# Kernel tuning notes

Hardware: AMD Instinct MI355X
Metric: run time of the kernel (lower is better)

Reference implementation:

```python
import jax, jax.numpy as jnp
import numpy as np

EPS = 1e-5
INF = 1e9
H, D = 16, 24  # no_heads, c_hidden

def layer_norm(x, w, b):
    mu = jnp.mean(x, axis=-1, keepdims=True)
    var = jnp.mean(jnp.square(x - mu), axis=-1, keepdims=True)
    return (x - mu) * jax.lax.rsqrt(var + EPS) * w + b

def setup_inputs() -> dict:
    key = jax.random.key(0)
    ks = jax.random.split(key, 12)
    B, N, Cq, Cz = 1, 1024, 384, 128
    s = 0.02
    return {
        "a": jax.random.normal(ks[0], (B, N, Cq), jnp.float32),
        "z": jax.random.normal(ks[1], (B, N, N, Cz), jnp.float32),
        "mask": jnp.ones((B, N), jnp.float32),
        "ln_a_w": jnp.ones((Cq,), jnp.float32),
        "ln_a_b": jnp.zeros((Cq,), jnp.float32),
        "ln_z_w": jnp.ones((Cz,), jnp.float32),
        "ln_z_b": jnp.zeros((Cz,), jnp.float32),
        "w_z": jax.random.normal(ks[2], (Cz, H), jnp.float32) * s,
        "wq": jax.random.normal(ks[3], (Cq, H * D), jnp.float32) * s,
        "wk": jax.random.normal(ks[4], (Cq, H * D), jnp.float32) * s,
        "wv": jax.random.normal(ks[5], (Cq, H * D), jnp.float32) * s,
        "wg": jax.random.normal(ks[6], (Cq, H * D), jnp.float32) * s,
        "bg": jnp.ones((H * D,), jnp.float32),
        "wo": jax.random.normal(ks[7], (H * D, Cq), jnp.float32) * s,
        "bo": jnp.zeros((Cq,), jnp.float32),
    }

def reference(a, z, mask, ln_a_w, ln_a_b, ln_z_w, ln_z_b, w_z, wq, wk, wv, wg, bg, wo, bo):
    B, N, Cq = a.shape
    a_ln = layer_norm(a, ln_a_w, ln_a_b)                      # [B,N,Cq]
    # pair bias: LN -> Linear(no bias) -> permute to [B,H,N,N]
    zb = layer_norm(z, ln_z_w, ln_z_b) @ w_z                  # [B,N,N,H]
    pair_bias = jnp.transpose(zb, (0, 3, 1, 2))               # [B,H,N,N]
    mask_bias = (INF * (mask - 1.0))[:, None, None, :]        # [B,1,1,N]
    q = (a_ln @ wq).reshape(B, N, H, D) * (D ** -0.5)
    k = (a_ln @ wk).reshape(B, N, H, D)
    v = (a_ln @ wv).reshape(B, N, H, D)
    logits = jnp.einsum("bqhd,bkhd->bhqk", q, k) + mask_bias + pair_bias
    attn = jax.nn.softmax(logits, axis=-1)
    o = jnp.einsum("bhqk,bkhd->bqhd", attn, v)                # [B,N,H,D]
    g = jax.nn.sigmoid(a_ln @ wg + bg).reshape(B, N, H, D)
    o = (g * o).reshape(B, N, H * D)
    return o @ wo + bo
```

## Files before the change

kernel.cpp:

```cpp
#include <hip/hip_runtime.h>
#include <hip/hip_bf16.h>

typedef float f32x4 __attribute__((ext_vector_type(4)));
typedef short s16x8 __attribute__((ext_vector_type(8)));

__device__ __forceinline__ unsigned short f2bf(float x){
  unsigned u = __float_as_uint(x);
  u += 0x7fffu + ((u >> 16) & 1u);
  return (unsigned short)(u >> 16);
}
__device__ __forceinline__ float bf2f(unsigned short h){
  return __uint_as_float(((unsigned)h) << 16);
}
__device__ __forceinline__ unsigned pk_bf(float a, float b){
  __hip_bfloat162 t = __float22bfloat162_rn(make_float2(a, b));
  return *reinterpret_cast<unsigned*>(&t);
}

__global__ __launch_bounds__(256) void prep_kernel(const float* __restrict__ a, const float* __restrict__ ln_a_w,
                             const float* __restrict__ ln_a_b, const float* __restrict__ lnzw,
                             const float* __restrict__ lnzb, const float* __restrict__ w_z,
                             const float* __restrict__ wq, const float* __restrict__ wk,
                             const float* __restrict__ wv, const float* __restrict__ wg,
                             const float* __restrict__ wo,
                             unsigned short* __restrict__ a_lnB, unsigned short* __restrict__ wBall,
                             unsigned short* __restrict__ wwB, float* __restrict__ TU,
                             unsigned short* __restrict__ qTp, unsigned short* __restrict__ kTp,
                             unsigned short* __restrict__ vTt){
  int bid = blockIdx.x, tid = threadIdx.x;
  if (bid < 180){
    __shared__ float t[64][65];
    int mat = bid/36, tt = bid - mat*36;
    int c0 = (tt % 6)*64, k0 = (tt / 6)*64;
    const float* src = mat == 0 ? wq : mat == 1 ? wk : mat == 2 ? wv : mat == 3 ? wg : wo;
    int r = tid >> 4, c4 = (tid & 15)*4;
    #pragma unroll
    for (int rr = 0; rr < 4; ++rr){
      float4 v = *(const float4*)(src + (size_t)(k0 + r + rr*16)*384 + c0 + c4);
      t[r + rr*16][c4+0] = v.x; t[r + rr*16][c4+1] = v.y;
      t[r + rr*16][c4+2] = v.z; t[r + rr*16][c4+3] = v.w;
    }
    __syncthreads();
    float scale = (mat == 0) ? 0.20412414523193154f : 1.f;
    int cc = tid >> 2, kp = (tid & 3)*16;
    unsigned ow[8];
    #pragma unroll
    for (int j = 0; j < 8; ++j)
      ow[j] = pk_bf(t[kp + 2*j][cc]*scale, t[kp + 2*j + 1][cc]*scale);
    unsigned short* dst = wBall + ((size_t)(mat*384 + c0 + cc)*384 + k0 + kp);
    *(uint4*)dst       = make_uint4(ow[0], ow[1], ow[2], ow[3]);
    *(uint4*)(dst + 8) = make_uint4(ow[4], ow[5], ow[6], ow[7]);
  } else if (bid < 436){
    int r = (bid - 180)*4 + (tid >> 6), l = tid & 63;
    const float* ap = a + (size_t)r*384;
    float x[6]; float s = 0.f, sq = 0.f;
    #pragma unroll
    for (int i = 0; i < 6; ++i){ x[i] = ap[i*64 + l]; s += x[i]; sq += x[i]*x[i]; }
    #pragma unroll
    for (int off = 32; off; off >>= 1){ s += __shfl_xor(s, off); sq += __shfl_xor(sq, off); }
    float mu = s*(1.f/384.f);
    float var = sq*(1.f/384.f) - mu*mu;
    float rs = rsqrtf(var + 1e-5f);
    #pragma unroll
    for (int i = 0; i < 6; ++i){ int c = i*64 + l; a_lnB[(size_t)r*384 + c] = f2bf((x[i]-mu)*rs*ln_a_w[c] + ln_a_b[c]); }
  } else if (bid == 436){
    if (tid < 128){
      float lw = lnzw[tid];
      #pragma unroll
      for (int h = 0; h < 16; ++h) wwB[tid*16 + h] = f2bf(lw * w_z[tid*16 + h]);
    }
    if (tid < 16){
      float T = 0.f, U = 0.f;
      for (int c = 0; c < 128; ++c){ T += lnzw[c]*w_z[c*16 + tid]; U += lnzb[c]*w_z[c*16 + tid]; }
      TU[tid] = T; TU[16 + tid] = U;
    }
  } else {
    int t = (bid - 437)*256 + tid;
    uint4 zv = make_uint4(0,0,0,0);
    if (t < 16384)      *(uint4*)(qTp + (size_t)t*32 + 24) = zv;
    else if (t < 32768) *(uint4*)(kTp + (size_t)(t - 16384)*32 + 24) = zv;
    else {
      int t2 = t - 32768;
      int h = t2 >> 10, w = t2 & 1023;
      *(uint4*)(vTt + ((size_t)h*32 + 24)*1024 + (size_t)w*8) = zv;
    }
  }
}

__global__ __launch_bounds__(256) void qkvg_kernel(const unsigned short* __restrict__ AB,
                                                   const unsigned short* __restrict__ wBt,
                                                   const float* __restrict__ bg,
                                                   unsigned short* __restrict__ qTp, unsigned short* __restrict__ kTp,
                                                   unsigned short* __restrict__ vTt, float* __restrict__ g){
  __shared__ short Al[64*8*8];
  __shared__ short Bl[64*8*8];
  int tid = threadIdx.x;
  int wave = tid >> 6, lane = tid & 63, l15 = lane & 15, sub = lane >> 4;
  int n0 = blockIdx.x*64, m0 = blockIdx.y*64;
  f32x4 acc[4];
  #pragma unroll
  for (int c = 0; c < 4; ++c) acc[c] = (f32x4){0.f,0.f,0.f,0.f};
  const s16x8* Ag = (const s16x8*)AB;
  const s16x8* Bg = (const s16x8*)wBt;
  s16x8* Al8 = (s16x8*)Al; s16x8* Bl8 = (s16x8*)Bl;
  for (int ks = 0; ks < 6; ++ks){
    int k0u = ks*8;
    #pragma unroll
    for (int j = 0; j < 2; ++j){
      int idx = tid*2 + j;
      int row = idx >> 3, u = idx & 7;
      Al8[row*8 + (u ^ (row & 7))] = Ag[(size_t)(m0 + row)*48 + k0u + u];
      Bl8[row*8 + (u ^ (row & 7))] = Bg[(size_t)(n0 + row)*48 + k0u + u];
    }
    __syncthreads();
    #pragma unroll
    for (int kk = 0; kk < 2; ++kk){
      int arow = wave*16 + l15;
      s16x8 af = Al8[arow*8 + ((kk*4 + sub) ^ (arow & 7))];
      #pragma unroll
      for (int c = 0; c < 4; ++c){
        int brow = c*16 + l15;
        s16x8 bf = Bl8[brow*8 + ((kk*4 + sub) ^ (brow & 7))];
        acc[c] = __builtin_amdgcn_mfma_f32_16x16x32_bf16(af, bf, acc[c], 0, 0, 0);
      }
    }
    __syncthreads();
  }
  int which = blockIdx.x / 6;
  int cb = n0 - which*384;
  if (which == 3){
    #pragma unroll
    for (int c = 0; c < 4; ++c){
      int col = cb + c*16 + l15;
      #pragma unroll
      for (int r = 0; r < 4; ++r){
        int row = m0 + wave*16 + sub*4 + r;
        float t = acc[c][r] + bg[col];
        g[(size_t)row*384 + col] = 1.f/(1.f + __expf(-t));
      }
    }
  } else if (which == 2){
    #pragma unroll
    for (int c = 0; c < 4; ++c){
      int col = cb + c*16 + l15;
      int h = col/24, d = col - h*24;
      unsigned p0 = pk_bf(acc[c][0], acc[c][1]);
      unsigned p1 = pk_bf(acc[c][2], acc[c][3]);
      size_t base = ((size_t)h*32 + d)*1024 + (size_t)(m0 + wave*16 + sub*4);
      *(uint2*)(vTt + base) = make_uint2(p0, p1);
    }
  } else {
    unsigned short* dst = which == 0 ? qTp : kTp;
    #pragma unroll
    for (int c = 0; c < 4; ++c){
      int col = cb + c*16 + l15;
      int h = col/24, d = col - h*24;
      #pragma unroll
      for (int r = 0; r < 4; ++r){
        int row = m0 + wave*16 + sub*4 + r;
        dst[((size_t)(h << 10) + row)*32 + d] = f2bf(acc[c][r]);
      }
    }
  }
}

__global__ __launch_bounds__(256) void zbias_kernel(const float* __restrict__ z, const unsigned short* __restrict__ wwB,
                                                    const float* __restrict__ TU, const float* __restrict__ mask,
                                                    unsigned short* __restrict__ pbM){
  __shared__ float sums[64];
  __shared__ float sqs[64];
  __shared__ float accT[64][17];
  int tid = threadIdx.x;
  int wave = tid >> 6, lane = tid & 63;
  int h = lane & 15, sub = lane >> 4;
  s16x8 bfr[4];
  #pragma unroll
  for (int kc = 0; kc < 4; ++kc)
    #pragma unroll
    for (int j = 0; j < 8; ++j) bfr[kc][j] = (short)wwB[(kc*32 + sub*8 + j)*16 + h];
  s16x8 ones1;
  #pragma unroll
  for (int j = 0; j < 8; ++j) ones1[j] = (h == 0) ? (short)0x3F80 : (short)0;
  int eh = tid >> 4, epl0 = (tid & 15)*4;
  float Te = TU[eh], Ue = TU[16 + eh];
  int row = wave*16 + h;
  for (int it = 0; it < 4; ++it){
    int tile = blockIdx.x + it*4096;
    size_t pairBase = (size_t)tile*64;
    const float* zrow = z + (pairBase + row)*128;
    f32x4 acc  = {0.f, 0.f, 0.f, 0.f};
    f32x4 accS = {0.f, 0.f, 0.f, 0.f};
    f32x4 accG = {0.f, 0.f, 0.f, 0.f};
    #pragma unroll
    for (int kc = 0; kc < 4; ++kc){
      f32x4 v0 = *(const f32x4*)(zrow + kc*32 + sub*8);
      f32x4 v1 = *(const f32x4*)(zrow + kc*32 + sub*8 + 4);
      union { unsigned u[4]; s16x8 s; } cv;
      cv.u[0] = pk_bf(v0.x, v0.y); cv.u[1] = pk_bf(v0.z, v0.w);
      cv.u[2] = pk_bf(v1.x, v1.y); cv.u[3] = pk_bf(v1.z, v1.w);
      s16x8 af = cv.s;
      acc  = __builtin_amdgcn_mfma_f32_16x16x32_bf16(af, bfr[kc], acc, 0, 0, 0);
      accS = __builtin_amdgcn_mfma_f32_16x16x32_bf16(af, ones1, accS, 0, 0, 0);
      accG = __builtin_amdgcn_mfma_f32_16x16x32_bf16(af, af, accG, 0, 0, 0);
    }
    #pragma unroll
    for (int r = 0; r < 4; ++r) accT[wave*16 + sub*4 + r][h] = acc[r];
    if (h == 0){
      #pragma unroll
      for (int r = 0; r < 4; ++r) sums[wave*16 + sub*4 + r] = accS[r];
    }
    if (sub == (h >> 2)){
      int r = h & 3;
      float vq = r == 0 ? accG[0] : r == 1 ? accG[1] : r == 2 ? accG[2] : accG[3];
      sqs[wave*16 + h] = vq;
    }
    __syncthreads();
    float mus[4], rss[4];
    #pragma unroll
    for (int rr = 0; rr < 4; ++rr){
      float mu = sums[epl0+rr]*(1.f/128.f);
      float var = sqs[epl0+rr]*(1.f/128.f) - mu*mu;
      mus[rr] = mu; rss[rr] = rsqrtf(var + 1e-5f);
    }
    size_t p0 = pairBase + epl0;
    int q = (int)(p0 >> 10), k0 = (int)(p0 & 1023);
    float4 mk = *(const float4*)(mask + k0);
    float bv[4];
    bv[0] = rss[0]*(accT[epl0+0][eh] - mus[0]*Te) + Ue + 1e9f*(mk.x - 1.f);
    bv[1] = rss[1]*(accT[epl0+1][eh] - mus[1]*Te) + Ue + 1e9f*(mk.y - 1.f);
    bv[2] = rss[2]*(accT[epl0+2][eh] - mus[2]*Te) + Ue + 1e9f*(mk.z - 1.f);
    bv[3] = rss[3]*(accT[epl0+3][eh] - mus[3]*Te) + Ue + 1e9f*(mk.w - 1.f);
    int qb = q >> 6, q64 = q & 63;
    int qg = q64 >> 4, subq = (q64 >> 2) & 3, rr = q64 & 3;
    int kkt = k0 >> 6, c = (k0 >> 4) & 3, l15k = k0 & 15;
    size_t cbase = ((((size_t)(eh*16 + qb)*16 + kkt)*4 + qg)*4 + c)*256 + (size_t)rr;
    #pragma unroll
    for (int i = 0; i < 4; ++i)
      pbM[cbase + (size_t)(subq*16 + l15k + i)*4] = f2bf(bv[i]);
    __syncthreads();
  }
}

__global__ __launch_bounds__(512) void attn_kernel(const unsigned short* __restrict__ qTp, const unsigned short* __restrict__ kTp,
                                                   const unsigned short* __restrict__ vTt, const unsigned short* __restrict__ pbM,
                                                   const float* __restrict__ g, unsigned short* __restrict__ ogB){
  __shared__ float lds[8192];
  int tid = threadIdx.x;
  int wave = tid >> 6, lane = tid & 63, l15 = lane & 15, sub = lane >> 4;
  int qb = blockIdx.x, h = blockIdx.y;
  int qg = wave & 3, half = wave >> 2;
  int qrow = qb*64 + qg*16 + l15;
  s16x8 qf = *(const s16x8*)(qTp + ((size_t)(h << 10) + qrow)*32 + sub*8);
  f32x4 o0 = {0.f,0.f,0.f,0.f}, o1 = {0.f,0.f,0.f,0.f};
  float m[4] = {-1e30f,-1e30f,-1e30f,-1e30f}, l[4] = {0.f,0.f,0.f,0.f};
  char* Pb = (char*)(lds + wave*1024);
  const unsigned short* kBase = kTp + ((size_t)(h << 10))*32;
  const unsigned short* vBase = vTt + (size_t)h*32*1024;
  const unsigned short* pbW = pbM + (size_t)(h*16 + qb)*16*4096 + (size_t)qg*1024 + (size_t)lane*4;
  for (int t = 0; t < 8; ++t){
    int kkt = half*8 + t;
    int kk0 = kkt*64;
    f32x4 s[4];
    #pragma unroll
    for (int c = 0; c < 4; ++c){
      s16x8 kf = *(const s16x8*)(kBase + (size_t)(kk0 + c*16 + l15)*32 + sub*8);
      s[c] = __builtin_amdgcn_mfma_f32_16x16x32_bf16(qf, kf, (f32x4){0.f,0.f,0.f,0.f}, 0, 0, 0);
    }
    const unsigned short* pbt = pbW + (size_t)kkt*4096;
    #pragma unroll
    for (int c = 0; c < 4; ++c){
      uint2 pv = *(const uint2*)(pbt + c*256);
      s[c][0] += bf2f((unsigned short)(pv.x & 0xffff));
      s[c][1] += bf2f((unsigned short)(pv.x >> 16));
      s[c][2] += bf2f((unsigned short)(pv.y & 0xffff));
      s[c][3] += bf2f((unsigned short)(pv.y >> 16));
    }
    #pragma unroll
    for (int r = 0; r < 4; ++r){
      float pm = fmaxf(fmaxf(s[0][r], s[1][r]), fmaxf(s[2][r], s[3][r]));
      pm = fmaxf(pm, __shfl_xor(pm, 1));
      pm = fmaxf(pm, __shfl_xor(pm, 2));
      pm = fmaxf(pm, __shfl_xor(pm, 4));
      pm = fmaxf(pm, __shfl_xor(pm, 8));
      float mn = fmaxf(m[r], pm);
      float corr = __expf(m[r] - mn);
      m[r] = mn;
      float ps = 0.f;
      #pragma unroll
      for (int c = 0; c < 4; ++c){ s[c][r] = __expf(s[c][r] - mn); ps += s[c][r]; }
      ps += __shfl_xor(ps, 1); ps += __shfl_xor(ps, 2);
      ps += __shfl_xor(ps, 4); ps += __shfl_xor(ps, 8);
      l[r] = l[r]*corr + ps;
      o0[r] *= corr; o1[r] *= corr;
    }
    #pragma unroll
    for (int c = 0; c < 4; ++c){
      #pragma unroll
      for (int r = 0; r < 4; ++r){
        int qq = sub*4 + r;
        int byte = ((qq*128 + (c*16 + l15)*2)) ^ ((qq & 7) << 4);
        *(short*)(Pb + byte) = (short)f2bf(s[c][r]);
      }
    }
    #pragma unroll
    for (int kh = 0; kh < 2; ++kh){
      int byteA = (l15*128 + kh*64 + sub*16) ^ ((l15 & 7) << 4);
      s16x8 pa = *(const s16x8*)(Pb + byteA);
      s16x8 vb0 = *(const s16x8*)(vBase + (size_t)l15*1024 + kk0 + kh*32 + sub*8);
      s16x8 vb1 = *(const s16x8*)(vBase + (size_t)(16 + l15)*1024 + kk0 + kh*32 + sub*8);
      o0 = __builtin_amdgcn_mfma_f32_16x16x32_bf16(pa, vb0, o0, 0, 0, 0);
      o1 = __builtin_amdgcn_mfma_f32_16x16x32_bf16(pa, vb1, o1, 0, 0, 0);
    }
  }
  {
    float* cw = lds + wave*1024 + lane*16;
    cw[0] = o0[0]; cw[1] = o0[1]; cw[2] = o0[2]; cw[3] = o0[3];
    cw[4] = o1[0]; cw[5] = o1[1]; cw[6] = o1[2]; cw[7] = o1[3];
    cw[8] = m[0]; cw[9] = m[1]; cw[10] = m[2]; cw[11] = m[3];
    cw[12] = l[0]; cw[13] = l[1]; cw[14] = l[2]; cw[15] = l[3];
  }
  __syncthreads();
  if (wave < 4){
    const float* c2 = lds + (wave + 4)*1024 + lane*16;
    #pragma unroll
    for (int r = 0; r < 4; ++r){
      float m2 = c2[8 + r], l2 = c2[12 + r];
      float nm = fmaxf(m[r], m2);
      float f1 = __expf(m[r] - nm), f2 = __expf(m2 - nm);
      float L = l[r]*f1 + l2*f2;
      float O0 = o0[r]*f1 + c2[r]*f2;
      float O1 = o1[r]*f1 + c2[4 + r]*f2;
      float inv = 1.f/L;
      int q = qb*64 + qg*16 + sub*4 + r;
      size_t base = (size_t)q*384 + h*24;
      ogB[base + l15] = f2bf(g[base + l15]*O0*inv);
      if (l15 < 8) ogB[base + 16 + l15] = f2bf(g[base + 16 + l15]*O1*inv);
    }
  }
}

__global__ __launch_bounds__(256) void gemm_out(const unsigned short* __restrict__ AB,
                                                const unsigned short* __restrict__ wBo,
                                                const float* __restrict__ bo, float* __restrict__ dst){
  __shared__ short Al[64*8*8];
  __shared__ short Bl[64*8*8];
  int tid = threadIdx.x;
  int wave = tid >> 6, lane = tid & 63, l15 = lane & 15, sub = lane >> 4;
  int n0 = blockIdx.x*64, m0 = blockIdx.y*64;
  f32x4 acc[4];
  #pragma unroll
  for (int c = 0; c < 4; ++c) acc[c] = (f32x4){0.f,0.f,0.f,0.f};
  const s16x8* Ag = (const s16x8*)AB;
  const s16x8* Bg = (const s16x8*)wBo;
  s16x8* Al8 = (s16x8*)Al; s16x8* Bl8 = (s16x8*)Bl;
  for (int ks = 0; ks < 6; ++ks){
    int k0u = ks*8;
    #pragma unroll
    for (int j = 0; j < 2; ++j){
      int idx = tid*2 + j;
      int row = idx >> 3, u = idx & 7;
      Al8[row*8 + (u ^ (row & 7))] = Ag[(size_t)(m0 + row)*48 + k0u + u];
      Bl8[row*8 + (u ^ (row & 7))] = Bg[(size_t)(n0 + row)*48 + k0u + u];
    }
    __syncthreads();
    #pragma unroll
    for (int kk = 0; kk < 2; ++kk){
      int arow = wave*16 + l15;
      s16x8 af = Al8[arow*8 + ((kk*4 + sub) ^ (arow & 7))];
      #pragma unroll
      for (int c = 0; c < 4; ++c){
        int brow = c*16 + l15;
        s16x8 bf = Bl8[brow*8 + ((kk*4 + sub) ^ (brow & 7))];
        acc[c] = __builtin_amdgcn_mfma_f32_16x16x32_bf16(af, bf, acc[c], 0, 0, 0);
      }
    }
    __syncthreads();
  }
  #pragma unroll
  for (int c = 0; c < 4; ++c){
    int col = n0 + c*16 + l15;
    float b = bo[col];
    #pragma unroll
    for (int r = 0; r < 4; ++r){
      int row = m0 + wave*16 + sub*4 + r;
      dst[(size_t)row*384 + col] = acc[c][r] + b;
    }
  }
}

extern "C" void kernel_launch(void* const* d_in, const int* in_sizes, int n_in,
                              void* d_out, int out_size, void* d_ws, size_t ws_size,
                              hipStream_t stream){
  const float* a      = (const float*)d_in[0];
  const float* z      = (const float*)d_in[1];
  const float* mask   = (const float*)d_in[2];
  const float* ln_a_w = (const float*)d_in[3];
  const float* ln_a_b = (const float*)d_in[4];
  const float* ln_z_w = (const float*)d_in[5];
  const float* ln_z_b = (const float*)d_in[6];
  const float* w_z    = (const float*)d_in[7];
  const float* wq     = (const float*)d_in[8];
  const float* wk     = (const float*)d_in[9];
  const float* wv     = (const float*)d_in[10];
  const float* wg     = (const float*)d_in[11];
  const float* bg     = (const float*)d_in[12];
  const float* wo     = (const float*)d_in[13];
  const float* bo     = (const float*)d_in[14];

  char* ws = (char*)d_ws;
  unsigned short* a_lnB = (unsigned short*)(ws + ((size_t)0u));
  unsigned short* wBall = (unsigned short*)(ws + ((size_t)1u << 20));
  unsigned short* qTp   = (unsigned short*)(ws + ((size_t)4u << 20));
  unsigned short* kTp   = (unsigned short*)(ws + ((size_t)6u << 20));
  unsigned short* vTt   = (unsigned short*)(ws + ((size_t)8u << 20));
  float* g    = (float*)(ws + ((size_t)10u << 20));
  unsigned short* ogB = (unsigned short*)(ws + ((size_t)12u << 20));
  unsigned short* wwB = (unsigned short*)(ws + ((size_t)14u << 20));
  float* TU   = (float*)(ws + ((size_t)14u << 20) + 8192);
  unsigned short* pbM = (unsigned short*)(ws + ((size_t)24u << 20));

  hipLaunchKernelGGL(prep_kernel, dim3(629), dim3(256), 0, stream, a, ln_a_w, ln_a_b,
                     ln_z_w, ln_z_b, w_z, wq, wk, wv, wg, wo, a_lnB, wBall, wwB, TU, qTp, kTp, vTt);
  hipLaunchKernelGGL(qkvg_kernel, dim3(24,16), dim3(256), 0, stream, a_lnB, wBall, bg, qTp, kTp, vTt, g);
  hipLaunchKernelGGL(zbias_kernel, dim3(4096), dim3(256), 0, stream, z, wwB, TU, mask, pbM);
  hipLaunchKernelGGL(attn_kernel, dim3(16,16), dim3(512), 0, stream, qTp, kTp, vTt, pbM, g, ogB);
  hipLaunchKernelGGL(gemm_out, dim3(6,16), dim3(256), 0, stream, ogB, wBall + (size_t)4*384*384, bo, (float*)d_out);
}
```

Baseline: 173.9 us.

## Merge QKVG GEMM and pair-bias kernels; split attention over more blocks

The QKVG projection GEMM and the z pair-bias kernel now run as one launch, with block index ranges picking the role, so the two independent stages can overlap and one launch is saved. The attention kernel now uses 32-row query blocks with four key-range splits per block instead of 64-row blocks with two splits, doubling the grid to fill more CUs. It also issues the pair-bias loads before the QK MFMAs. The cost is a longer serial three-way merge of partial softmax state in the first wave group.

```diff
diff --git a/kernel.cpp b/kernel.cpp
--- a/kernel.cpp
+++ b/kernel.cpp
@@ -87,157 +87,158 @@
   }
 }
 
-__global__ __launch_bounds__(256) void qkvg_kernel(const unsigned short* __restrict__ AB,
-                                                   const unsigned short* __restrict__ wBt,
-                                                   const float* __restrict__ bg,
-                                                   unsigned short* __restrict__ qTp, unsigned short* __restrict__ kTp,
-                                                   unsigned short* __restrict__ vTt, float* __restrict__ g){
-  __shared__ short Al[64*8*8];
-  __shared__ short Bl[64*8*8];
-  int tid = threadIdx.x;
+__global__ __launch_bounds__(256) void midfuse_kernel(const unsigned short* __restrict__ AB,
+                                                      const unsigned short* __restrict__ wBt,
+                                                      const float* __restrict__ bg,
+                                                      unsigned short* __restrict__ qTp, unsigned short* __restrict__ kTp,
+                                                      unsigned short* __restrict__ vTt, float* __restrict__ g,
+                                                      const float* __restrict__ z, const unsigned short* __restrict__ wwB,
+                                                      const float* __restrict__ TU, const float* __restrict__ mask,
+                                                      unsigned short* __restrict__ pbM){
+  __shared__ char smem[16384];
+  int bid = blockIdx.x, tid = threadIdx.x;
   int wave = tid >> 6, lane = tid & 63, l15 = lane & 15, sub = lane >> 4;
-  int n0 = blockIdx.x*64, m0 = blockIdx.y*64;
-  f32x4 acc[4];
-  #pragma unroll
-  for (int c = 0; c < 4; ++c) acc[c] = (f32x4){0.f,0.f,0.f,0.f};
-  const s16x8* Ag = (const s16x8*)AB;
-  const s16x8* Bg = (const s16x8*)wBt;
-  s16x8* Al8 = (s16x8*)Al; s16x8* Bl8 = (s16x8*)Bl;
-  for (int ks = 0; ks < 6; ++ks){
-    int k0u = ks*8;
-    #pragma unroll
-    for (int j = 0; j < 2; ++j){
-      int idx = tid*2 + j;
-      int row = idx >> 3, u = idx & 7;
-      Al8[row*8 + (u ^ (row & 7))] = Ag[(size_t)(m0 + row)*48 + k0u + u];
-      Bl8[row*8 + (u ^ (row & 7))] = Bg[(size_t)(n0 + row)*48 + k0u + u];
-    }
-    __syncthreads();
-    #pragma unroll
-    for (int kk = 0; kk < 2; ++kk){
-      int arow = wave*16 + l15;
-      s16x8 af = Al8[arow*8 + ((kk*4 + sub) ^ (arow & 7))];
+  if (bid < 384){
+    s16x8* Al8 = (s16x8*)smem;
+    s16x8* Bl8 = (s16x8*)(smem + 8192);
+    int bx = bid % 24, by = bid / 24;
+    int n0 = bx*64, m0 = by*64;
+    f32x4 acc[4];
+    #pragma unroll
+    for (int c = 0; c < 4; ++c) acc[c] = (f32x4){0.f,0.f,0.f,0.f};
+    const s16x8* Ag = (const s16x8*)AB;
+    const s16x8* Bg = (const s16x8*)wBt;
+    for (int ks = 0; ks < 6; ++ks){
+      int k0u = ks*8;
+      #pragma unroll
+      for (int j = 0; j < 2; ++j){
+        int idx = tid*2 + j;
+        int row = idx >> 3, u = idx & 7;
+        Al8[row*8 + (u ^ (row & 7))] = Ag[(size_t)(m0 + row)*48 + k0u + u];
+        Bl8[row*8 + (u ^ (row & 7))] = Bg[(size_t)(n0 + row)*48 + k0u + u];
+      }
+      __syncthreads();
+      #pragma unroll
+      for (int kk = 0; kk < 2; ++kk){
+        int arow = wave*16 + l15;
+        s16x8 af = Al8[arow*8 + ((kk*4 + sub) ^ (arow & 7))];
+        #pragma unroll
+        for (int c = 0; c < 4; ++c){
+          int brow = c*16 + l15;
+          s16x8 bf = Bl8[brow*8 + ((kk*4 + sub) ^ (brow & 7))];
+          acc[c] = __builtin_amdgcn_mfma_f32_16x16x32_bf16(af, bf, acc[c], 0, 0, 0);
+        }
+      }
+      __syncthreads();
+    }
+    int which = bx / 6;
+    int cb = n0 - which*384;
+    if (which == 3){
       #pragma unroll
       for (int c = 0; c < 4; ++c){
-        int brow = c*16 + l15;
-        s16x8 bf = Bl8[brow*8 + ((kk*4 + sub) ^ (brow & 7))];
-        acc[c] = __builtin_amdgcn_mfma_f32_16x16x32_bf16(af, bf, acc[c], 0, 0, 0);
-      }
-    }
-    __syncthreads();
-  }
-  int which = blockIdx.x / 6;
-  int cb = n0 - which*384;
-  if (which == 3){
-    #pragma unroll
-    for (int c = 0; c < 4; ++c){
-      int col = cb + c*16 + l15;
-      #pragma unroll
-      for (int r = 0; r < 4; ++r){
-        int row = m0 + wave*16 + sub*4 + r;
-        float t = acc[c][r] + bg[col];
-        g[(size_t)row*384 + col] = 1.f/(1.f + __expf(-t));
-      }
-    }
-  } else if (which == 2){
-    #pragma unroll
-    for (int c = 0; c < 4; ++c){
-      int col = cb + c*16 + l15;
-      int h = col/24, d = col - h*24;
-      unsigned p0 = pk_bf(acc[c][0], acc[c][1]);
-      unsigned p1 = pk_bf(acc[c][2], acc[c][3]);
-      size_t base = ((size_t)h*32 + d)*1024 + (size_t)(m0 + wave*16 + sub*4);
-      *(uint2*)(vTt + base) = make_uint2(p0, p1);
+        int col = cb + c*16 + l15;
+        #pragma unroll
+        for (int r = 0; r < 4; ++r){
+          int row = m0 + wave*16 + sub*4 + r;
+          float t = acc[c][r] + bg[col];
+          g[(size_t)row*384 + col] = 1.f/(1.f + __expf(-t));
+        }
+      }
+    } else if (which == 2){
+      #pragma unroll
+      for (int c = 0; c < 4; ++c){
+        int col = cb + c*16 + l15;
+        int h = col/24, d = col - h*24;
+        unsigned p0 = pk_bf(acc[c][0], acc[c][1]);
+        unsigned p1 = pk_bf(acc[c][2], acc[c][3]);
+        size_t base = ((size_t)h*32 + d)*1024 + (size_t)(m0 + wave*16 + sub*4);
+        *(uint2*)(vTt + base) = make_uint2(p0, p1);
+      }
+    } else {
+      unsigned short* dst = which == 0 ? qTp : kTp;
+      #pragma unroll
+      for (int c = 0; c < 4; ++c){
+        int col = cb + c*16 + l15;
+        int h = col/24, d = col - h*24;
+        #pragma unroll
+        for (int r = 0; r < 4; ++r){
+          int row = m0 + wave*16 + sub*4 + r;
+          dst[((size_t)(h << 10) + row)*32 + d] = f2bf(acc[c][r]);
+        }
+      }
     }
   } else {
-    unsigned short* dst = which == 0 ? qTp : kTp;
-    #pragma unroll
-    for (int c = 0; c < 4; ++c){
-      int col = cb + c*16 + l15;
-      int h = col/24, d = col - h*24;
-      #pragma unroll
-      for (int r = 0; r < 4; ++r){
-        int row = m0 + wave*16 + sub*4 + r;
-        dst[((size_t)(h << 10) + row)*32 + d] = f2bf(acc[c][r]);
-      }
-    }
-  }
-}
-
-__global__ __launch_bounds__(256) void zbias_kernel(const float* __restrict__ z, const unsigned short* __restrict__ wwB,
-                                                    const float* __restrict__ TU, const float* __restrict__ mask,
-                                                    unsigned short* __restrict__ pbM){
-  __shared__ float sums[64];
-  __shared__ float sqs[64];
-  __shared__ float accT[64][17];
-  int tid = threadIdx.x;
-  int wave = tid >> 6, lane = tid & 63;
-  int h = lane & 15, sub = lane >> 4;
-  s16x8 bfr[4];
-  #pragma unroll
-  for (int kc = 0; kc < 4; ++kc)
-    #pragma unroll
-    for (int j = 0; j < 8; ++j) bfr[kc][j] = (short)wwB[(kc*32 + sub*8 + j)*16 + h];
-  s16x8 ones1;
-  #pragma unroll
-  for (int j = 0; j < 8; ++j) ones1[j] = (h == 0) ? (short)0x3F80 : (short)0;
-  int eh = tid >> 4, epl0 = (tid & 15)*4;
-  float Te = TU[eh], Ue = TU[16 + eh];
-  int row = wave*16 + h;
-  for (int it = 0; it < 4; ++it){
-    int tile = blockIdx.x + it*4096;
-    size_t pairBase = (size_t)tile*64;
-    const float* zrow = z + (pairBase + row)*128;
-    f32x4 acc  = {0.f, 0.f, 0.f, 0.f};
-    f32x4 accS = {0.f, 0.f, 0.f, 0.f};
-    f32x4 accG = {0.f, 0.f, 0.f, 0.f};
-    #pragma unroll
-    for (int kc = 0; kc < 4; ++kc){
-      f32x4 v0 = *(const f32x4*)(zrow + kc*32 + sub*8);
-      f32x4 v1 = *(const f32x4*)(zrow + kc*32 + sub*8 + 4);
-      union { unsigned u[4]; s16x8 s; } cv;
-      cv.u[0] = pk_bf(v0.x, v0.y); cv.u[1] = pk_bf(v0.z, v0.w);
-      cv.u[2] = pk_bf(v1.x, v1.y); cv.u[3] = pk_bf(v1.z, v1.w);
-      s16x8 af = cv.s;
-      acc  = __builtin_amdgcn_mfma_f32_16x16x32_bf16(af, bfr[kc], acc, 0, 0, 0);
-      accS = __builtin_amdgcn_mfma_f32_16x16x32_bf16(af, ones1, accS, 0, 0, 0);
-      accG = __builtin_amdgcn_mfma_f32_16x16x32_bf16(af, af, accG, 0, 0, 0);
-    }
-    #pragma unroll
-    for (int r = 0; r < 4; ++r) accT[wave*16 + sub*4 + r][h] = acc[r];
-    if (h == 0){
-      #pragma unroll
-      for (int r = 0; r < 4; ++r) sums[wave*16 + sub*4 + r] = accS[r];
-    }
-    if (sub == (h >> 2)){
-      int r = h & 3;
-      float vq = r == 0 ? accG[0] : r == 1 ? accG[1] : r == 2 ? accG[2] : accG[3];
-      sqs[wave*16 + h] = vq;
-    }
-    __syncthreads();
-    float mus[4], rss[4];
-    #pragma unroll
-    for (int rr = 0; rr < 4; ++rr){
-      float mu = sums[epl0+rr]*(1.f/128.f);
-      float var = sqs[epl0+rr]*(1.f/128.f) - mu*mu;
-      mus[rr] = mu; rss[rr] = rsqrtf(var + 1e-5f);
-    }
-    size_t p0 = pairBase + epl0;
-    int q = (int)(p0 >> 10), k0 = (int)(p0 & 1023);
-    float4 mk = *(const float4*)(mask + k0);
-    float bv[4];
-    bv[0] = rss[0]*(accT[epl0+0][eh] - mus[0]*Te) + Ue + 1e9f*(mk.x - 1.f);
-    bv[1] = rss[1]*(accT[epl0+1][eh] - mus[1]*Te) + Ue + 1e9f*(mk.y - 1.f);
-    bv[2] = rss[2]*(accT[epl0+2][eh] - mus[2]*Te) + Ue + 1e9f*(mk.z - 1.f);
-    bv[3] = rss[3]*(accT[epl0+3][eh] - mus[3]*Te) + Ue + 1e9f*(mk.w - 1.f);
-    int qb = q >> 6, q64 = q & 63;
-    int qg = q64 >> 4, subq = (q64 >> 2) & 3, rr = q64 & 3;
-    int kkt = k0 >> 6, c = (k0 >> 4) & 3, l15k = k0 & 15;
-    size_t cbase = ((((size_t)(eh*16 + qb)*16 + kkt)*4 + qg)*4 + c)*256 + (size_t)rr;
-    #pragma unroll
-    for (int i = 0; i < 4; ++i)
-      pbM[cbase + (size_t)(subq*16 + l15k + i)*4] = f2bf(bv[i]);
-    __syncthreads();
+    float* sums = (float*)smem;
+    float* sqs  = sums + 64;
+    float (*accT)[17] = (float(*)[17])(sqs + 64);
+    int tb = bid - 384;
+    int h = l15, subz = sub;
+    s16x8 bfr[4];
+    #pragma unroll
+    for (int kc = 0; kc < 4; ++kc)
+      #pragma unroll
+      for (int j = 0; j < 8; ++j) bfr[kc][j] = (short)wwB[(kc*32 + subz*8 + j)*16 + h];
+    s16x8 ones1;
+    #pragma unroll
+    for (int j = 0; j < 8; ++j) ones1[j] = (h == 0) ? (short)0x3F80 : (short)0;
+    int eh = tid >> 4, epl0 = (tid & 15)*4;
+    float Te = TU[eh], Ue = TU[16 + eh];
+    int row = wave*16 + h;
+    for (int it = 0; it < 4; ++it){
+      int tile = tb + it*4096;
+      size_t pairBase = (size_t)tile*64;
+      const float* zrow = z + (pairBase + row)*128;
+      f32x4 acc  = {0.f, 0.f, 0.f, 0.f};
+      f32x4 accS = {0.f, 0.f, 0.f, 0.f};
+      f32x4 accG = {0.f, 0.f, 0.f, 0.f};
+      #pragma unroll
+      for (int kc = 0; kc < 4; ++kc){
+        f32x4 v0 = *(const f32x4*)(zrow + kc*32 + subz*8);
+        f32x4 v1 = *(const f32x4*)(zrow + kc*32 + subz*8 + 4);
+        union { unsigned u[4]; s16x8 s; } cv;
+        cv.u[0] = pk_bf(v0.x, v0.y); cv.u[1] = pk_bf(v0.z, v0.w);
+        cv.u[2] = pk_bf(v1.x, v1.y); cv.u[3] = pk_bf(v1.z, v1.w);
+        s16x8 af = cv.s;
+        acc  = __builtin_amdgcn_mfma_f32_16x16x32_bf16(af, bfr[kc], acc, 0, 0, 0);
+        accS = __builtin_amdgcn_mfma_f32_16x16x32_bf16(af, ones1, accS, 0, 0, 0);
+        accG = __builtin_amdgcn_mfma_f32_16x16x32_bf16(af, af, accG, 0, 0, 0);
+      }
+      #pragma unroll
+      for (int r = 0; r < 4; ++r) accT[wave*16 + subz*4 + r][h] = acc[r];
+      if (h == 0){
+        #pragma unroll
+        for (int r = 0; r < 4; ++r) sums[wave*16 + subz*4 + r] = accS[r];
+      }
+      if (subz == (h >> 2)){
+        int r = h & 3;
+        float vq = r == 0 ? accG[0] : r == 1 ? accG[1] : r == 2 ? accG[2] : accG[3];
+        sqs[wave*16 + h] = vq;
+      }
+      __syncthreads();
+      float mus[4], rss[4];
+      #pragma unroll
+      for (int rr = 0; rr < 4; ++rr){
+        float mu = sums[epl0+rr]*(1.f/128.f);
+        float var = sqs[epl0+rr]*(1.f/128.f) - mu*mu;
+        mus[rr] = mu; rss[rr] = rsqrtf(var + 1e-5f);
+      }
+      size_t p0 = pairBase + epl0;
+      int q = (int)(p0 >> 10), k0 = (int)(p0 & 1023);
+      float4 mk = *(const float4*)(mask + k0);
+      float bv[4];
+      bv[0] = rss[0]*(accT[epl0+0][eh] - mus[0]*Te) + Ue + 1e9f*(mk.x - 1.f);
+      bv[1] = rss[1]*(accT[epl0+1][eh] - mus[1]*Te) + Ue + 1e9f*(mk.y - 1.f);
+      bv[2] = rss[2]*(accT[epl0+2][eh] - mus[2]*Te) + Ue + 1e9f*(mk.z - 1.f);
+      bv[3] = rss[3]*(accT[epl0+3][eh] - mus[3]*Te) + Ue + 1e9f*(mk.w - 1.f);
+      int qb = q >> 6, q64 = q & 63;
+      int qg = q64 >> 4, subq = (q64 >> 2) & 3, rr2 = q64 & 3;
+      int kkt = k0 >> 6, c = (k0 >> 4) & 3, l15k = k0 & 15;
+      size_t cbase = ((((size_t)(eh*16 + qb)*16 + kkt)*4 + qg)*4 + c)*256 + (size_t)rr2;
+      #pragma unroll
+      for (int i = 0; i < 4; ++i)
+        pbM[cbase + (size_t)(subq*16 + l15k + i)*4] = f2bf(bv[i]);
+      __syncthreads();
+    }
   }
 }
 
@@ -247,33 +248,40 @@
   __shared__ float lds[8192];
   int tid = threadIdx.x;
   int wave = tid >> 6, lane = tid & 63, l15 = lane & 15, sub = lane >> 4;
-  int qb = blockIdx.x, h = blockIdx.y;
-  int qg = wave & 3, half = wave >> 2;
-  int qrow = qb*64 + qg*16 + l15;
+  int qb32 = blockIdx.x, h = blockIdx.y;
+  int qg_l = wave & 1, kkq = wave >> 1;
+  int qrow = qb32*32 + qg_l*16 + l15;
   s16x8 qf = *(const s16x8*)(qTp + ((size_t)(h << 10) + qrow)*32 + sub*8);
   f32x4 o0 = {0.f,0.f,0.f,0.f}, o1 = {0.f,0.f,0.f,0.f};
   float m[4] = {-1e30f,-1e30f,-1e30f,-1e30f}, l[4] = {0.f,0.f,0.f,0.f};
   char* Pb = (char*)(lds + wave*1024);
   const unsigned short* kBase = kTp + ((size_t)(h << 10))*32;
   const unsigned short* vBase = vTt + (size_t)h*32*1024;
-  const unsigned short* pbW = pbM + (size_t)(h*16 + qb)*16*4096 + (size_t)qg*1024 + (size_t)lane*4;
-  for (int t = 0; t < 8; ++t){
-    int kkt = half*8 + t;
+  int qb64 = qb32 >> 1, qg4 = (qb32 & 1)*2 + qg_l;
+  const unsigned short* pbW = pbM + (size_t)(h*16 + qb64)*16*4096 + (size_t)qg4*1024 + (size_t)lane*4;
+  for (int t = 0; t < 4; ++t){
+    int kkt = kkq*4 + t;
     int kk0 = kkt*64;
+    const unsigned short* pbt = pbW + (size_t)kkt*4096;
+    uint2 pv0 = *(const uint2*)(pbt + 0);
+    uint2 pv1 = *(const uint2*)(pbt + 256);
+    uint2 pv2 = *(const uint2*)(pbt + 512);
+    uint2 pv3 = *(const uint2*)(pbt + 768);
     f32x4 s[4];
     #pragma unroll
     for (int c = 0; c < 4; ++c){
       s16x8 kf = *(const s16x8*)(kBase + (size_t)(kk0 + c*16 + l15)*32 + sub*8);
       s[c] = __builtin_amdgcn_mfma_f32_16x16x32_bf16(qf, kf, (f32x4){0.f,0.f,0.f,0.f}, 0, 0, 0);
     }
-    const unsigned short* pbt = pbW + (size_t)kkt*4096;
-    #pragma unroll
-    for (int c = 0; c < 4; ++c){
-      uint2 pv = *(const uint2*)(pbt + c*256);
-      s[c][0] += bf2f((unsigned short)(pv.x & 0xffff));
-      s[c][1] += bf2f((unsigned short)(pv.x >> 16));
-      s[c][2] += bf2f((unsigned short)(pv.y & 0xffff));
-      s[c][3] += bf2f((unsigned short)(pv.y >> 16));
+    {
+      uint2 pv[4] = {pv0, pv1, pv2, pv3};
+      #pragma unroll
+      for (int c = 0; c < 4; ++c){
+        s[c][0] += bf2f((unsigned short)(pv[c].x & 0xffff));
+        s[c][1] += bf2f((unsigned short)(pv[c].x >> 16));
+        s[c][2] += bf2f((unsigned short)(pv[c].y & 0xffff));
+        s[c][3] += bf2f((unsigned short)(pv[c].y >> 16));
+      }
     }
     #pragma unroll
     for (int r = 0; r < 4; ++r){
@@ -320,21 +328,28 @@
     cw[12] = l[0]; cw[13] = l[1]; cw[14] = l[2]; cw[15] = l[3];
   }
   __syncthreads();
-  if (wave < 4){
-    const float* c2 = lds + (wave + 4)*1024 + lane*16;
+  if (kkq == 0){
+    #pragma unroll
+    for (int k2 = 1; k2 < 4; ++k2){
+      const float* c2 = lds + (size_t)(k2*2 + qg_l)*1024 + lane*16;
+      #pragma unroll
+      for (int r = 0; r < 4; ++r){
+        float m2 = c2[8 + r], l2 = c2[12 + r];
+        float nm = fmaxf(m[r], m2);
+        float f1 = __expf(m[r] - nm), f2 = __expf(m2 - nm);
+        l[r] = l[r]*f1 + l2*f2;
+        o0[r] = o0[r]*f1 + c2[r]*f2;
+        o1[r] = o1[r]*f1 + c2[4 + r]*f2;
+        m[r] = nm;
+      }
+    }
     #pragma unroll
     for (int r = 0; r < 4; ++r){
-      float m2 = c2[8 + r], l2 = c2[12 + r];
-      float nm = fmaxf(m[r], m2);
-      float f1 = __expf(m[r] - nm), f2 = __expf(m2 - nm);
-      float L = l[r]*f1 + l2*f2;
-      float O0 = o0[r]*f1 + c2[r]*f2;
-      float O1 = o1[r]*f1 + c2[4 + r]*f2;
-      float inv = 1.f/L;
-      int q = qb*64 + qg*16 + sub*4 + r;
+      float inv = 1.f/l[r];
+      int q = qb32*32 + qg_l*16 + sub*4 + r;
       size_t base = (size_t)q*384 + h*24;
-      ogB[base + l15] = f2bf(g[base + l15]*O0*inv);
-      if (l15 < 8) ogB[base + 16 + l15] = f2bf(g[base + 16 + l15]*O1*inv);
+      ogB[base + l15] = f2bf(g[base + l15]*o0[r]*inv);
+      if (l15 < 8) ogB[base + 16 + l15] = f2bf(g[base + 16 + l15]*o1[r]*inv);
     }
   }
 }
@@ -421,8 +436,8 @@
 
   hipLaunchKernelGGL(prep_kernel, dim3(629), dim3(256), 0, stream, a, ln_a_w, ln_a_b,
                      ln_z_w, ln_z_b, w_z, wq, wk, wv, wg, wo, a_lnB, wBall, wwB, TU, qTp, kTp, vTt);
-  hipLaunchKernelGGL(qkvg_kernel, dim3(24,16), dim3(256), 0, stream, a_lnB, wBall, bg, qTp, kTp, vTt, g);
-  hipLaunchKernelGGL(zbias_kernel, dim3(4096), dim3(256), 0, stream, z, wwB, TU, mask, pbM);
-  hipLaunchKernelGGL(attn_kernel, dim3(16,16), dim3(512), 0, stream, qTp, kTp, vTt, pbM, g, ogB);
+  hipLaunchKernelGGL(midfuse_kernel, dim3(4480), dim3(256), 0, stream, a_lnB, wBall, bg,
+                     qTp, kTp, vTt, g, z, wwB, TU, mask, pbM);
+  hipLaunchKernelGGL(attn_kernel, dim3(32,16), dim3(512), 0, stream, qTp, kTp, vTt, pbM, g, ogB);
   hipLaunchKernelGGL(gemm_out, dim3(6,16), dim3(256), 0, stream, ogB, wBall + (size_t)4*384*384, bo, (float*)d_out);
 }
```

Result: no change. 173.6 us (-0.2%).
